# Performance work log

Measured on AMD Instinct MI355X. Metric: run time of the kernel, lower is better.

The kernel has to match this reference:

```python
import jax, jax.numpy as jnp
import numpy as np

B, T, D = 16, 4096, 1024
UNITS = 1024


def setup_inputs() -> dict:
    key = jax.random.key(0)
    ks = jax.random.split(key, 8)
    s_in = 1.0 / np.sqrt(D)
    s_u = 1.0 / np.sqrt(UNITS)
    return {
        "hidden_state": jax.random.normal(ks[0], (B, D), jnp.float32),
        "encoder_output": jax.random.normal(ks[1], (B, T, D), jnp.float32),
        "W1": jax.random.normal(ks[2], (D, UNITS), jnp.float32) * s_in,
        "b1": jnp.zeros((UNITS,), jnp.float32),
        "W2": jax.random.normal(ks[3], (D, UNITS), jnp.float32) * s_in,
        "b2": jnp.zeros((UNITS,), jnp.float32),
        "V": jax.random.normal(ks[4], (UNITS, 1), jnp.float32) * s_u,
        "bv": jnp.zeros((1,), jnp.float32),
    }


def reference(hidden_state, encoder_output, W1, b1, W2, b2, V, bv):
    # Bahdanau additive attention: score = V(tanh(W1(h) + W2(enc)))
    h_proj = hidden_state @ W1 + b1                      # [B, U]
    e_proj = jnp.einsum("btd,du->btu", encoder_output, W2) + b2  # [B, T, U]
    feat = jnp.tanh(h_proj[:, None, :] + e_proj)          # [B, T, U]
    score = feat @ V + bv                                 # [B, T, 1]
    attention_weights = jax.nn.softmax(score, axis=1)     # [B, T, 1]
    context_vector = jnp.sum(attention_weights * encoder_output, axis=1)  # [B, D]
    return context_vector, attention_weights
```

## Files before the change

### kernel.cpp

```cpp
#include <hip/hip_runtime.h>
#include <hip/hip_bf16.h>
#include <math.h>

#define B_ 16
#define T_ 4096
#define D_ 1024
#define U_ 1024
#define M_ (B_*T_)

typedef __attribute__((ext_vector_type(8))) short short8;
typedef __attribute__((ext_vector_type(4))) short short4v;
typedef __attribute__((ext_vector_type(4))) float float4v;

static __device__ __forceinline__ short f2bf(float f) {
    unsigned u = __builtin_bit_cast(unsigned, f);
    u += 0x7FFFu + ((u >> 16) & 1u);
    return (short)(u >> 16);
}
static __device__ __forceinline__ short bfc(float f) {
    __hip_bfloat16 b = __float2bfloat16(f);
    return (short)__builtin_bit_cast(unsigned short, b);
}
static __device__ __forceinline__ short8 cvt8(float4v lo, float4v hi) {
    short8 r;
    r[0]=bfc(lo[0]); r[1]=bfc(lo[1]); r[2]=bfc(lo[2]); r[3]=bfc(lo[3]);
    r[4]=bfc(hi[0]); r[5]=bfc(hi[1]); r[6]=bfc(hi[2]); r[7]=bfc(hi[3]);
    return r;
}
static __device__ __forceinline__ float fast_tanh(float x) {
    float c = fminf(fmaxf(2.f * x, -30.f), 30.f);
    float t = __expf(c);
    return __fdividef(t - 1.f, t + 1.f);
}

#define GLLDS(GP, LP) __builtin_amdgcn_global_load_lds( \
    (const __attribute__((address_space(1))) void*)(GP), \
    (__attribute__((address_space(3))) void*)(LP), 16, 0, 0)

__global__ void prep_fused(const float* __restrict__ h, const float* __restrict__ W1,
                           const float* __restrict__ b1, const float* __restrict__ b2,
                           const float* __restrict__ W2,
                           float* __restrict__ hbp, short* __restrict__ W2T) {
    int bx = blockIdx.x;
    if (bx < 256) {
        int kc = bx >> 6;
        int gid = (bx & 63) * 256 + threadIdx.x;
        int b = gid >> 10, u = gid & 1023;
        const float* hr = h + b * D_ + kc * 256;
        const float* w = W1 + (size_t)(kc * 256) * U_ + u;
        float s0 = 0.f, s1 = 0.f, s2 = 0.f, s3 = 0.f;
        for (int k = 0; k < 256; k += 4) {
            s0 += hr[k+0] * w[(size_t)(k+0) * U_];
            s1 += hr[k+1] * w[(size_t)(k+1) * U_];
            s2 += hr[k+2] * w[(size_t)(k+2) * U_];
            s3 += hr[k+3] * w[(size_t)(k+3) * U_];
        }
        float s = ((s0 + s1) + (s2 + s3));
        if (kc == 0) s += b1[u] + b2[u];
        hbp[kc * 16384 + gid] = s;
    } else {
        __shared__ short t[64][65];
        int x = bx - 256;
        int k0 = (x >> 4) * 64, u0 = (x & 15) * 64;
        int tx = threadIdx.x & 63, ty = threadIdx.x >> 6;
        #pragma unroll
        for (int r = 0; r < 16; ++r) {
            int kk = ty * 16 + r;
            t[kk][tx] = f2bf(W2[(size_t)(k0 + kk) * U_ + u0 + tx]);
        }
        __syncthreads();
        #pragma unroll
        for (int r = 0; r < 16; ++r) {
            int uu = ty * 16 + r;
            W2T[(size_t)(u0 + uu) * D_ + k0 + tx] = t[tx][uu];
        }
    }
}

__global__ __launch_bounds__(512, 2) void gemm_score_8ph(
    const float* __restrict__ encf,
    const short* __restrict__ W2T,
    const float* __restrict__ hbp,
    const float* __restrict__ V,
    float* __restrict__ scorepart)
{
    __shared__ __align__(16) short lds[65536];

    const int tid = threadIdx.x;
    const int g = blockIdx.x;
    const int c = g & 7, q = g >> 3;
    const int ntile = q & 3;
    const int mtile = (q >> 2) * 8 + c;
    const int row0 = mtile * 256, n0 = ntile * 256;
    const int bidx = row0 >> 12;

    const int lane = tid & 63;
    const int wv = tid >> 6;
    const int wm = wv >> 2, wn = wv & 3;
    const int lm = lane & 15, quad = lane >> 4;

    const int srow32 = tid >> 4;
    const int scol = (((tid & 15) ^ (srow32 & 15)) << 2);
    const float* aSrc = encf + (size_t)(row0 + srow32) * D_ + scol;
    char* aDst = (char*)lds + tid * 16;

#define STG_A32(kt, R) do { \
    GLLDS(aSrc + (size_t)(R) * D_ + (kt) * 64,        aDst + (R) * 256); \
    GLLDS(aSrc + (size_t)((R) + 32) * D_ + (kt) * 64, aDst + (R) * 256 + 8192); \
} while (0)

    const int srowB = tid >> 3;
    const int lslotB = (tid & 7) ^ (srowB & 7);
    const short* bS = W2T + (size_t)(n0 + srowB) * D_ + lslotB * 8;
    short* bD = lds + 32768 + tid * 8;
#define STG_B(kt, h, bf) do { \
    GLLDS(bS + (size_t)((h) * 128) * D_ + (kt) * 64,      bD + (bf) * 16384 + (h) * 8192); \
    GLLDS(bS + (size_t)((h) * 128 + 64) * D_ + (kt) * 64, bD + (bf) * 16384 + (h) * 8192 + 4096); \
} while (0)
#define LDS_RD(off) (*(const short8*)(lds + (off)))
#define MFMA(a, b, c) __builtin_amdgcn_mfma_f32_16x16x32_bf16((a), (b), (c), 0, 0, 0)
#define LDA_FRAG(d0, d1, rw) do { \
    const int _r = (rw); \
    const int _k = _r & 15; \
    const char* _base = (const char*)lds + _r * 256; \
    float4v _a = *(const float4v*)(_base + ((((2 * quad)     ^ _k) ) << 4)); \
    float4v _b = *(const float4v*)(_base + ((((2 * quad + 1) ^ _k) ) << 4)); \
    float4v _c = *(const float4v*)(_base + ((((2 * quad + 8) ^ _k) ) << 4)); \
    float4v _d = *(const float4v*)(_base + ((((2 * quad + 9) ^ _k) ) << 4)); \
    d0 = cvt8(_a, _b); d1 = cvt8(_c, _d); \
} while (0)

    const int bB0 = 32768 + (wn * 64 + lm) * 64 + (quad ^ (lm & 7)) * 8;
    const int bB1 = bB0 ^ 32;

    float4v acc[8][4] = {};
    short8 Af[4][2], Bf[4][2];

    STG_B(0, 0, 0); STG_B(0, 1, 0);
    STG_A32(0, 0); STG_A32(0, 128);
    STG_A32(0, 64); STG_A32(0, 192);
    STG_B(1, 0, 1); STG_B(1, 1, 1);
    asm volatile("s_waitcnt vmcnt(8)" ::: "memory");
    __builtin_amdgcn_s_barrier();
    __builtin_amdgcn_sched_barrier(0);

    for (int t = 0; t < 16; ++t) {
        const int bufS = (t & 1) * 16384;
        #pragma unroll
        for (int mi = 0; mi < 4; ++mi)
            LDA_FRAG(Af[mi][0], Af[mi][1], wm * 128 + mi * 16 + lm);
        #pragma unroll
        for (int ni = 0; ni < 2; ++ni) {
            Bf[ni][0] = LDS_RD(bufS + bB0 + ni * 1024);
            Bf[ni][1] = LDS_RD(bufS + bB1 + ni * 1024);
        }
        __builtin_amdgcn_s_barrier();
        __builtin_amdgcn_s_setprio(1);
        #pragma unroll
        for (int mi = 0; mi < 4; ++mi)
            #pragma unroll
            for (int ni = 0; ni < 2; ++ni) {
                acc[mi][ni] = MFMA(Af[mi][0], Bf[ni][0], acc[mi][ni]);
                acc[mi][ni] = MFMA(Af[mi][1], Bf[ni][1], acc[mi][ni]);
            }
        __builtin_amdgcn_s_setprio(0);
        __builtin_amdgcn_s_barrier();
        #pragma unroll
        for (int ni = 0; ni < 2; ++ni) {
            Bf[2 + ni][0] = LDS_RD(bufS + bB0 + (2 + ni) * 1024);
            Bf[2 + ni][1] = LDS_RD(bufS + bB1 + (2 + ni) * 1024);
        }
        if (t < 15) { STG_A32(t + 1, 0); STG_A32(t + 1, 128); }
        __builtin_amdgcn_s_barrier();
        __builtin_amdgcn_s_setprio(1);
        #pragma unroll
        for (int mi = 0; mi < 4; ++mi)
            #pragma unroll
            for (int ni = 0; ni < 2; ++ni) {
                acc[mi][2 + ni] = MFMA(Af[mi][0], Bf[2 + ni][0], acc[mi][2 + ni]);
                acc[mi][2 + ni] = MFMA(Af[mi][1], Bf[2 + ni][1], acc[mi][2 + ni]);
            }
        __builtin_amdgcn_s_setprio(0);
        if (t < 15) { asm volatile("s_waitcnt vmcnt(6)" ::: "memory"); }
        else        { asm volatile("s_waitcnt vmcnt(0)" ::: "memory"); }
        __builtin_amdgcn_s_barrier();
        #pragma unroll
        for (int mi = 0; mi < 4; ++mi)
            LDA_FRAG(Af[mi][0], Af[mi][1], wm * 128 + 64 + mi * 16 + lm);
        if (t < 14) STG_B(t + 2, 0, t & 1);
        __builtin_amdgcn_s_barrier();
        __builtin_amdgcn_s_setprio(1);
        #pragma unroll
        for (int mi = 0; mi < 4; ++mi)
            #pragma unroll
            for (int ni = 0; ni < 2; ++ni) {
                acc[4 + mi][ni] = MFMA(Af[mi][0], Bf[ni][0], acc[4 + mi][ni]);
                acc[4 + mi][ni] = MFMA(Af[mi][1], Bf[ni][1], acc[4 + mi][ni]);
            }
        __builtin_amdgcn_s_setprio(0);
        __builtin_amdgcn_s_barrier();
        if (t < 15) { STG_A32(t + 1, 64); STG_A32(t + 1, 192); }
        if (t < 14) STG_B(t + 2, 1, t & 1);
        __builtin_amdgcn_s_barrier();
        __builtin_amdgcn_s_setprio(1);
        #pragma unroll
        for (int mi = 0; mi < 4; ++mi)
            #pragma unroll
            for (int ni = 0; ni < 2; ++ni) {
                acc[4 + mi][2 + ni] = MFMA(Af[mi][0], Bf[2 + ni][0], acc[4 + mi][2 + ni]);
                acc[4 + mi][2 + ni] = MFMA(Af[mi][1], Bf[2 + ni][1], acc[4 + mi][2 + ni]);
            }
        __builtin_amdgcn_s_setprio(0);
        if (t < 14)      { asm volatile("s_waitcnt vmcnt(8)" ::: "memory"); }
        else if (t == 14){ asm volatile("s_waitcnt vmcnt(4)" ::: "memory"); }
        __builtin_amdgcn_s_barrier();
        __builtin_amdgcn_sched_barrier(0);
    }

    float* sbuf = (float*)lds;
    float hbv[4], Vv[4];
    #pragma unroll
    for (int ni = 0; ni < 4; ++ni) {
        int U = n0 + wn * 64 + ni * 16 + lm;
        int o = bidx * U_ + U;
        hbv[ni] = hbp[o] + hbp[16384 + o] + hbp[32768 + o] + hbp[49152 + o];
        Vv[ni]  = V[U];
    }
    #pragma unroll
    for (int mi = 0; mi < 8; ++mi) {
        #pragma unroll
        for (int r = 0; r < 4; ++r) {
            float s = 0.f;
            #pragma unroll
            for (int ni = 0; ni < 4; ++ni)
                s += fast_tanh(acc[mi][ni][r] + hbv[ni]) * Vv[ni];
            #pragma unroll
            for (int off = 1; off < 16; off <<= 1)
                s += __shfl_xor(s, off, 64);
            if (lm == 0)
                sbuf[wn * 256 + wm * 128 + mi * 16 + quad * 4 + r] = s;
        }
    }
    __syncthreads();
    if (tid < 256)
        scorepart[(size_t)ntile * M_ + row0 + tid] =
            sbuf[tid] + sbuf[256 + tid] + sbuf[512 + tid] + sbuf[768 + tid];
}

__global__ __launch_bounds__(256) void ctx_softmax(
        const float* __restrict__ scorepart,
        const float* __restrict__ bv,
        const float* __restrict__ enc,
        float* __restrict__ out_attn,
        float* __restrict__ part)
{
    __shared__ float sm[T_];
    __shared__ float wsm[128];
    __shared__ float lacc[1024];
    __shared__ float red[8];
    const int x = blockIdx.x, tid = threadIdx.x;
    const int b = x & 15, tc = x >> 4;
    const int wvi = tid >> 6;
    const float bv0 = bv[0];
    float lmax = -1e30f;
    #pragma unroll
    for (int i = 0; i < 16; ++i) {
        int t = tid + i * 256;
        const float* sp = scorepart + (size_t)b * T_ + t;
        float s = bv0 + sp[0] + sp[M_] + sp[2 * (size_t)M_] + sp[3 * (size_t)M_];
        sm[t] = s;
        lmax = fmaxf(lmax, s);
    }
    #pragma unroll
    for (int off = 1; off < 64; off <<= 1) lmax = fmaxf(lmax, __shfl_xor(lmax, off, 64));
    if ((tid & 63) == 0) red[wvi] = lmax;
    __syncthreads();
    const float m = fmaxf(fmaxf(red[0], red[1]), fmaxf(red[2], red[3]));
    float lsum = 0.f;
    #pragma unroll
    for (int i = 0; i < 16; ++i) lsum += __expf(sm[tid + i * 256] - m);
    #pragma unroll
    for (int off = 1; off < 64; off <<= 1) lsum += __shfl_xor(lsum, off, 64);
    if ((tid & 63) == 0) red[4 + wvi] = lsum;
    __syncthreads();
    const float tot = (red[4] + red[5]) + (red[6] + red[7]);
    const float rinv = 1.f / tot;
    if ((tid >> 7) == (tc & 1)) {
        int j = tid & 127;
        int t = tc * 128 + j;
        float w = __expf(sm[t] - m) * rinv;
        wsm[j] = w;
        out_attn[b * T_ + t] = w;
    }
    __syncthreads();
    const int par = tid >> 7;
    const int d0 = (tid & 127) * 8;
    const float* e0 = enc + (size_t)(b * T_ + tc * 128 + par) * D_ + d0;
    float4v a0 = {}, a1 = {};
    #pragma unroll 4
    for (int it = 0; it < 64; ++it) {
        float4v v0 = *(const float4v*)(e0 + (size_t)it * 2 * D_);
        float4v v1 = *(const float4v*)(e0 + (size_t)it * 2 * D_ + 4);
        float w = wsm[it * 2 + par];
        a0[0] += w * v0[0]; a0[1] += w * v0[1];
        a0[2] += w * v0[2]; a0[3] += w * v0[3];
        a1[0] += w * v1[0]; a1[1] += w * v1[1];
        a1[2] += w * v1[2]; a1[3] += w * v1[3];
    }
    if (par) {
        *(float4v*)(lacc + (tid & 127) * 8)     = a0;
        *(float4v*)(lacc + (tid & 127) * 8 + 4) = a1;
    }
    __syncthreads();
    if (!par) {
        const float* l = lacc + tid * 8;
        a0[0] += l[0]; a0[1] += l[1]; a0[2] += l[2]; a0[3] += l[3];
        a1[0] += l[4]; a1[1] += l[5]; a1[2] += l[6]; a1[3] += l[7];
        float4v* pp = (float4v*)(part + (size_t)x * 1024 + tid * 8);
        pp[0] = a0; pp[1] = a1;
    }
}

__global__ void ctx_reduce_kernel(const float* __restrict__ part, float* __restrict__ ctx) {
    int gid = blockIdx.x * 256 + threadIdx.x;
    int b = gid >> 10, d = gid & 1023;
    float s = 0.f;
    #pragma unroll
    for (int tc = 0; tc < 32; ++tc) s += part[(size_t)(tc * 16 + b) * 1024 + d];
    ctx[gid] = s;
}

extern "C" void kernel_launch(void* const* d_in, const int* in_sizes, int n_in,
                              void* d_out, int out_size, void* d_ws, size_t ws_size,
                              hipStream_t stream) {
    const float* h   = (const float*)d_in[0];
    const float* enc = (const float*)d_in[1];
    const float* W1  = (const float*)d_in[2];
    const float* b1  = (const float*)d_in[3];
    const float* W2  = (const float*)d_in[4];
    const float* b2  = (const float*)d_in[5];
    const float* V   = (const float*)d_in[6];
    const float* bv  = (const float*)d_in[7];
    float* out = (float*)d_out;
    float* ws  = (float*)d_ws;

    float* hbp       = ws;
    float* scorepart = ws + 65536;
    short* W2T   = (short*)(ws + 65536 + 524288);
    float* ctxpart   = (float*)W2T;

    prep_fused<<<512, 256, 0, stream>>>(h, W1, b1, b2, W2, hbp, W2T);
    gemm_score_8ph<<<1024, 512, 0, stream>>>(enc, W2T, hbp, V, scorepart);
    ctx_softmax<<<512, 256, 0, stream>>>(scorepart, bv, enc, out + 16384, ctxpart);
    ctx_reduce_kernel<<<64, 256, 0, stream>>>(ctxpart, out);
}
```

Baseline: 547.5 us.

## Change GEMM wave tiling to 4x2 layout with simpler single-stage B prefetch

Rearranges the eight waves from a 2x4 grid (128 rows by 64 columns each) into a 4x2 grid (64 rows by 128 columns each). Each wave now loads its A fragments once per k-step and streams B fragments in four chunks. The B prefetch depth drops from two stages to one, with a full vmcnt(0) wait at each iteration end. This aims to cut the per-wave A conversion and LDS reads from fp32, at the cost of less latency hiding for global loads and more B LDS reads. The epilogue now reduces two column-wave partials per row instead of four.

```diff
diff --git a/kernel.cpp b/kernel.cpp
--- a/kernel.cpp
+++ b/kernel.cpp
@@ -96,7 +96,7 @@
 
     const int lane = tid & 63;
     const int wv = tid >> 6;
-    const int wm = wv >> 2, wn = wv & 3;
+    const int wm = wv >> 1, wn = wv & 1;
     const int lm = lane & 15, quad = lane >> 4;
 
     const int srow32 = tid >> 4;
@@ -130,17 +130,15 @@
     d0 = cvt8(_a, _b); d1 = cvt8(_c, _d); \
 } while (0)
 
-    const int bB0 = 32768 + (wn * 64 + lm) * 64 + (quad ^ (lm & 7)) * 8;
+    const int bB0 = 32768 + (wn * 128 + lm) * 64 + (quad ^ (lm & 7)) * 8;
     const int bB1 = bB0 ^ 32;
 
-    float4v acc[8][4] = {};
-    short8 Af[4][2], Bf[4][2];
+    float4v acc[4][8] = {};
+    short8 Af[4][2], Bf[2][2];
 
     STG_B(0, 0, 0); STG_B(0, 1, 0);
-    STG_A32(0, 0); STG_A32(0, 128);
-    STG_A32(0, 64); STG_A32(0, 192);
-    STG_B(1, 0, 1); STG_B(1, 1, 1);
-    asm volatile("s_waitcnt vmcnt(8)" ::: "memory");
+    STG_A32(0, 0); STG_A32(0, 64); STG_A32(0, 128); STG_A32(0, 192);
+    asm volatile("s_waitcnt vmcnt(0)" ::: "memory");
     __builtin_amdgcn_s_barrier();
     __builtin_amdgcn_sched_barrier(0);
 
@@ -148,103 +146,93 @@
         const int bufS = (t & 1) * 16384;
         #pragma unroll
         for (int mi = 0; mi < 4; ++mi)
-            LDA_FRAG(Af[mi][0], Af[mi][1], wm * 128 + mi * 16 + lm);
-        #pragma unroll
-        for (int ni = 0; ni < 2; ++ni) {
-            Bf[ni][0] = LDS_RD(bufS + bB0 + ni * 1024);
-            Bf[ni][1] = LDS_RD(bufS + bB1 + ni * 1024);
-        }
+            LDA_FRAG(Af[mi][0], Af[mi][1], wm * 64 + mi * 16 + lm);
+        Bf[0][0] = LDS_RD(bufS + bB0);        Bf[0][1] = LDS_RD(bufS + bB1);
+        Bf[1][0] = LDS_RD(bufS + bB0 + 1024); Bf[1][1] = LDS_RD(bufS + bB1 + 1024);
+        if (t < 15) { STG_B(t + 1, 0, (t + 1) & 1); STG_B(t + 1, 1, (t + 1) & 1); }
         __builtin_amdgcn_s_barrier();
         __builtin_amdgcn_s_setprio(1);
         #pragma unroll
-        for (int mi = 0; mi < 4; ++mi)
-            #pragma unroll
-            for (int ni = 0; ni < 2; ++ni) {
-                acc[mi][ni] = MFMA(Af[mi][0], Bf[ni][0], acc[mi][ni]);
-                acc[mi][ni] = MFMA(Af[mi][1], Bf[ni][1], acc[mi][ni]);
-            }
+        for (int mi = 0; mi < 4; ++mi) {
+            acc[mi][0] = MFMA(Af[mi][0], Bf[0][0], acc[mi][0]);
+            acc[mi][0] = MFMA(Af[mi][1], Bf[0][1], acc[mi][0]);
+            acc[mi][1] = MFMA(Af[mi][0], Bf[1][0], acc[mi][1]);
+            acc[mi][1] = MFMA(Af[mi][1], Bf[1][1], acc[mi][1]);
+        }
         __builtin_amdgcn_s_setprio(0);
         __builtin_amdgcn_s_barrier();
-        #pragma unroll
-        for (int ni = 0; ni < 2; ++ni) {
-            Bf[2 + ni][0] = LDS_RD(bufS + bB0 + (2 + ni) * 1024);
-            Bf[2 + ni][1] = LDS_RD(bufS + bB1 + (2 + ni) * 1024);
-        }
-        if (t < 15) { STG_A32(t + 1, 0); STG_A32(t + 1, 128); }
+        Bf[0][0] = LDS_RD(bufS + bB0 + 2048); Bf[0][1] = LDS_RD(bufS + bB1 + 2048);
+        Bf[1][0] = LDS_RD(bufS + bB0 + 3072); Bf[1][1] = LDS_RD(bufS + bB1 + 3072);
+        if (t < 15) { STG_A32(t + 1, 0); STG_A32(t + 1, 64); }
         __builtin_amdgcn_s_barrier();
         __builtin_amdgcn_s_setprio(1);
         #pragma unroll
-        for (int mi = 0; mi < 4; ++mi)
-            #pragma unroll
-            for (int ni = 0; ni < 2; ++ni) {
-                acc[mi][2 + ni] = MFMA(Af[mi][0], Bf[2 + ni][0], acc[mi][2 + ni]);
-                acc[mi][2 + ni] = MFMA(Af[mi][1], Bf[2 + ni][1], acc[mi][2 + ni]);
-            }
+        for (int mi = 0; mi < 4; ++mi) {
+            acc[mi][2] = MFMA(Af[mi][0], Bf[0][0], acc[mi][2]);
+            acc[mi][2] = MFMA(Af[mi][1], Bf[0][1], acc[mi][2]);
+            acc[mi][3] = MFMA(Af[mi][0], Bf[1][0], acc[mi][3]);
+            acc[mi][3] = MFMA(Af[mi][1], Bf[1][1], acc[mi][3]);
+        }
         __builtin_amdgcn_s_setprio(0);
-        if (t < 15) { asm volatile("s_waitcnt vmcnt(6)" ::: "memory"); }
-        else        { asm volatile("s_waitcnt vmcnt(0)" ::: "memory"); }
-        __builtin_amdgcn_s_barrier();
-        #pragma unroll
-        for (int mi = 0; mi < 4; ++mi)
-            LDA_FRAG(Af[mi][0], Af[mi][1], wm * 128 + 64 + mi * 16 + lm);
-        if (t < 14) STG_B(t + 2, 0, t & 1);
+        __builtin_amdgcn_s_barrier();
+        Bf[0][0] = LDS_RD(bufS + bB0 + 4096); Bf[0][1] = LDS_RD(bufS + bB1 + 4096);
+        Bf[1][0] = LDS_RD(bufS + bB0 + 5120); Bf[1][1] = LDS_RD(bufS + bB1 + 5120);
+        if (t < 15) { STG_A32(t + 1, 128); STG_A32(t + 1, 192); }
         __builtin_amdgcn_s_barrier();
         __builtin_amdgcn_s_setprio(1);
         #pragma unroll
-        for (int mi = 0; mi < 4; ++mi)
-            #pragma unroll
-            for (int ni = 0; ni < 2; ++ni) {
-                acc[4 + mi][ni] = MFMA(Af[mi][0], Bf[ni][0], acc[4 + mi][ni]);
-                acc[4 + mi][ni] = MFMA(Af[mi][1], Bf[ni][1], acc[4 + mi][ni]);
-            }
+        for (int mi = 0; mi < 4; ++mi) {
+            acc[mi][4] = MFMA(Af[mi][0], Bf[0][0], acc[mi][4]);
+            acc[mi][4] = MFMA(Af[mi][1], Bf[0][1], acc[mi][4]);
+            acc[mi][5] = MFMA(Af[mi][0], Bf[1][0], acc[mi][5]);
+            acc[mi][5] = MFMA(Af[mi][1], Bf[1][1], acc[mi][5]);
+        }
         __builtin_amdgcn_s_setprio(0);
         __builtin_amdgcn_s_barrier();
-        if (t < 15) { STG_A32(t + 1, 64); STG_A32(t + 1, 192); }
-        if (t < 14) STG_B(t + 2, 1, t & 1);
+        Bf[0][0] = LDS_RD(bufS + bB0 + 6144); Bf[0][1] = LDS_RD(bufS + bB1 + 6144);
+        Bf[1][0] = LDS_RD(bufS + bB0 + 7168); Bf[1][1] = LDS_RD(bufS + bB1 + 7168);
         __builtin_amdgcn_s_barrier();
         __builtin_amdgcn_s_setprio(1);
         #pragma unroll
-        for (int mi = 0; mi < 4; ++mi)
-            #pragma unroll
-            for (int ni = 0; ni < 2; ++ni) {
-                acc[4 + mi][2 + ni] = MFMA(Af[mi][0], Bf[2 + ni][0], acc[4 + mi][2 + ni]);
-                acc[4 + mi][2 + ni] = MFMA(Af[mi][1], Bf[2 + ni][1], acc[4 + mi][2 + ni]);
-            }
+        for (int mi = 0; mi < 4; ++mi) {
+            acc[mi][6] = MFMA(Af[mi][0], Bf[0][0], acc[mi][6]);
+            acc[mi][6] = MFMA(Af[mi][1], Bf[0][1], acc[mi][6]);
+            acc[mi][7] = MFMA(Af[mi][0], Bf[1][0], acc[mi][7]);
+            acc[mi][7] = MFMA(Af[mi][1], Bf[1][1], acc[mi][7]);
+        }
         __builtin_amdgcn_s_setprio(0);
-        if (t < 14)      { asm volatile("s_waitcnt vmcnt(8)" ::: "memory"); }
-        else if (t == 14){ asm volatile("s_waitcnt vmcnt(4)" ::: "memory"); }
+        if (t < 15) { asm volatile("s_waitcnt vmcnt(0)" ::: "memory"); }
         __builtin_amdgcn_s_barrier();
         __builtin_amdgcn_sched_barrier(0);
     }
 
     float* sbuf = (float*)lds;
-    float hbv[4], Vv[4];
-    #pragma unroll
-    for (int ni = 0; ni < 4; ++ni) {
-        int U = n0 + wn * 64 + ni * 16 + lm;
+    float hbv[8], Vv[8];
+    #pragma unroll
+    for (int ni = 0; ni < 8; ++ni) {
+        int U = n0 + wn * 128 + ni * 16 + lm;
         int o = bidx * U_ + U;
         hbv[ni] = hbp[o] + hbp[16384 + o] + hbp[32768 + o] + hbp[49152 + o];
         Vv[ni]  = V[U];
     }
     #pragma unroll
-    for (int mi = 0; mi < 8; ++mi) {
+    for (int mi = 0; mi < 4; ++mi) {
         #pragma unroll
         for (int r = 0; r < 4; ++r) {
             float s = 0.f;
             #pragma unroll
-            for (int ni = 0; ni < 4; ++ni)
+            for (int ni = 0; ni < 8; ++ni)
                 s += fast_tanh(acc[mi][ni][r] + hbv[ni]) * Vv[ni];
             #pragma unroll
             for (int off = 1; off < 16; off <<= 1)
                 s += __shfl_xor(s, off, 64);
             if (lm == 0)
-                sbuf[wn * 256 + wm * 128 + mi * 16 + quad * 4 + r] = s;
+                sbuf[wn * 256 + wm * 64 + mi * 16 + quad * 4 + r] = s;
         }
     }
     __syncthreads();
     if (tid < 256)
-        scorepart[(size_t)ntile * M_ + row0 + tid] =
-            sbuf[tid] + sbuf[256 + tid] + sbuf[512 + tid] + sbuf[768 + tid];
+        scorepart[(size_t)ntile * M_ + row0 + tid] = sbuf[tid] + sbuf[256 + tid];
 }
 
 __global__ __launch_bounds__(256) void ctx_softmax(
```

Result: slower. 561.0 us (+2.5%).
